# Kernel tuning notes

Measured on AMD Instinct MI355X. Metric: run time of the kernel, lower is better.

The kernel has to match this reference:

```python
import jax
import jax.numpy as jnp
from jax import lax
import numpy as np

NUM_OUTPUT_POINTS = 2048
NUM_NEIGHBORS = 32


def setup_inputs() -> dict:
    key = jax.random.key(0)
    k1, k2 = jax.random.split(key)
    coordinates = jax.random.normal(k1, (8, 8192, 3), dtype=jnp.float32)
    features = jax.random.normal(k2, (8, 8192, 128), dtype=jnp.float32)
    return {"coordinates": coordinates, "features": features}


def farthest_point_sample(coords, num_output_points):
    """Deterministic FPS (first point = index 0). coords: (B, N, D) -> idx (B, M) int32."""
    B, N, D = coords.shape

    def step(carry, _):
        dist, farthest = carry  # (B, N), (B,)
        centroid = jnp.take_along_axis(coords, farthest[:, None, None], axis=1)  # (B,1,D)
        cur = jnp.linalg.norm(coords - centroid, axis=-1)  # (B, N), L2 norm
        dist = jnp.minimum(dist, cur)
        new_far = jnp.argmax(dist, axis=-1).astype(jnp.int32)
        return (dist, new_far), farthest

    init = (jnp.full((B, N), 1e10, coords.dtype), jnp.zeros((B,), jnp.int32))
    _, idx = lax.scan(step, init, None, length=num_output_points)  # (M, B)
    return idx.T  # (B, M)


def knn_point(num_neighbors, coords, centers):
    """coords (B,N,D), centers (B,M,D) -> (B,M,K) indices of nearest neighbors (L2)."""
    # squared distances via expansion (avoids (B,M,N,D) diff tensor)
    c2 = jnp.sum(centers * centers, axis=-1, keepdims=True)        # (B,M,1)
    p2 = jnp.sum(coords * coords, axis=-1)[:, None, :]             # (B,1,N)
    d2 = c2 + p2 - 2.0 * jnp.einsum('bmd,bnd->bmn', centers, coords)
    _, nbr_idx = lax.top_k(-d2, num_neighbors)                     # smallest distances
    return nbr_idx


def _gather_points(points, idx):
    """points (B,N,C), idx (B,...) -> (B,...,C)."""
    return jax.vmap(lambda p, i: p[i])(points, idx)


def reference(coordinates, features):
    fps_idx = farthest_point_sample(coordinates, NUM_OUTPUT_POINTS)      # (B, M)
    out_coordinates = _gather_points(coordinates, fps_idx)               # (B, M, D)
    nbr_idx = knn_point(NUM_NEIGHBORS, coordinates, out_coordinates)     # (B, M, K)
    group_features = _gather_points(features, nbr_idx)                   # (B, M, K, C)
    out_features = jnp.mean(group_features, axis=2)                      # (B, M, C)
    return out_coordinates, out_features
```

## Files before the change

kernel.cpp:

```cpp
#include <hip/hip_runtime.h>

#define BB 8
#define NN 8192
#define MM 2048
#define KK 32
#define CC 128

#define FPS_T 512
#define FPS_P (NN / FPS_T)

template <int Ctrl, int RowMask>
__device__ __forceinline__ int dpp_i(int x) {
  return __builtin_amdgcn_update_dpp(x, x, Ctrl, RowMask, 0xf, false);
}

__device__ __forceinline__ float wave_max63(float v) {
  v = fmaxf(v, __int_as_float(dpp_i<0x111, 0xf>(__float_as_int(v))));
  v = fmaxf(v, __int_as_float(dpp_i<0x112, 0xf>(__float_as_int(v))));
  v = fmaxf(v, __int_as_float(dpp_i<0x114, 0xf>(__float_as_int(v))));
  v = fmaxf(v, __int_as_float(dpp_i<0x118, 0xf>(__float_as_int(v))));
  v = fmaxf(v, __int_as_float(dpp_i<0x142, 0xa>(__float_as_int(v))));
  v = fmaxf(v, __int_as_float(dpp_i<0x143, 0xc>(__float_as_int(v))));
  return v;
}

__device__ __forceinline__ unsigned int wave_minu63(unsigned int v) {
  unsigned int o;
  o = (unsigned int)dpp_i<0x111, 0xf>((int)v); v = o < v ? o : v;
  o = (unsigned int)dpp_i<0x112, 0xf>((int)v); v = o < v ? o : v;
  o = (unsigned int)dpp_i<0x114, 0xf>((int)v); v = o < v ? o : v;
  o = (unsigned int)dpp_i<0x118, 0xf>((int)v); v = o < v ? o : v;
  o = (unsigned int)dpp_i<0x142, 0xa>((int)v); v = o < v ? o : v;
  o = (unsigned int)dpp_i<0x143, 0xc>((int)v); v = o < v ? o : v;
  return v;
}

template <int Ctrl, int RowMask>
__device__ __forceinline__ unsigned long long dpp_u64(unsigned long long v) {
  const int lo = (int)(unsigned int)v;
  const int hi = (int)(unsigned int)(v >> 32);
  const unsigned int nlo = (unsigned int)dpp_i<Ctrl, RowMask>(lo);
  const unsigned int nhi = (unsigned int)dpp_i<Ctrl, RowMask>(hi);
  return ((unsigned long long)nhi << 32) | nlo;
}

__device__ __forceinline__ unsigned long long wave_minu64_63(unsigned long long v) {
  unsigned long long o;
  o = dpp_u64<0x111, 0xf>(v); v = o < v ? o : v;
  o = dpp_u64<0x112, 0xf>(v); v = o < v ? o : v;
  o = dpp_u64<0x114, 0xf>(v); v = o < v ? o : v;
  o = dpp_u64<0x118, 0xf>(v); v = o < v ? o : v;
  o = dpp_u64<0x142, 0xa>(v); v = o < v ? o : v;
  o = dpp_u64<0x143, 0xc>(v); v = o < v ? o : v;
  return v;
}

__global__ __launch_bounds__(FPS_T, 1)
void fps_kernel(const float* __restrict__ coords, float* __restrict__ out_coords) {
  const int b = blockIdx.x;
  const int t = threadIdx.x;
  const float* cb = coords + (size_t)b * NN * 3;

  __shared__ float s_x[NN], s_y[NN], s_z[NN];
  __shared__ float s_gpart[FPS_T / 64];
  __shared__ unsigned int s_ipart[FPS_T / 64];

  float x[FPS_P], y[FPS_P], z[FPS_P], d2m[FPS_P];
#pragma unroll
  for (int j = 0; j < FPS_P; ++j) {
    const int p = t + j * FPS_T;
    x[j] = cb[p * 3 + 0];
    y[j] = cb[p * 3 + 1];
    z[j] = cb[p * 3 + 2];
    d2m[j] = 1e20f;
    s_x[p] = x[j]; s_y[p] = y[j]; s_z[p] = z[j];
  }

  if (t == 0) {
    out_coords[(size_t)(b * MM) * 3 + 0] = cb[0];
    out_coords[(size_t)(b * MM) * 3 + 1] = cb[1];
    out_coords[(size_t)(b * MM) * 3 + 2] = cb[2];
  }
  float cx = cb[0], cy = cb[1], cz = cb[2];

  for (int it = 1; it < MM; ++it) {
    float bestv = -1.0f;
#pragma unroll
    for (int j = 0; j < FPS_P; ++j) {
      const float dx = __fsub_rn(x[j], cx);
      const float dy = __fsub_rn(y[j], cy);
      const float dz = __fsub_rn(z[j], cz);
      const float d2 = __fadd_rn(__fadd_rn(__fmul_rn(dx, dx), __fmul_rn(dy, dy)),
                                 __fmul_rn(dz, dz));
      const float nd = fminf(d2m[j], d2);
      d2m[j] = nd;
      bestv = fmaxf(bestv, nd);
    }

    const float wv = wave_max63(bestv);
    if ((t & 63) == 63) s_gpart[t >> 6] = wv;
    __syncthreads();
    float gmax = s_gpart[0];
#pragma unroll
    for (int w = 1; w < FPS_T / 64; ++w) gmax = fmaxf(gmax, s_gpart[w]);

    float lo_f;
    if (!(gmax > 0.0f)) {
      lo_f = 0.0f;
    } else {
      const float s = __fsqrt_rn(gmax);
      const float sp = __int_as_float(__float_as_int(s) - 1);
      const double mid = 0.5 * ((double)s + (double)sp);
      const double lod = mid * mid;
      float c = (float)lod;
      if ((double)c < lod) c = __int_as_float(__float_as_int(c) + 1);
      lo_f = c;
    }

    unsigned int mi = 0xFFFFFFFFu;
    if (bestv >= lo_f) {
#pragma unroll
      for (int j = 0; j < FPS_P; ++j) {
        const unsigned int pi = (unsigned int)(t + j * FPS_T);
        if (d2m[j] >= lo_f && pi < mi) mi = pi;
      }
    }
    const unsigned int wi = wave_minu63(mi);
    if ((t & 63) == 63) s_ipart[t >> 6] = wi;
    __syncthreads();
    unsigned int widx = s_ipart[0];
#pragma unroll
    for (int w = 1; w < FPS_T / 64; ++w) widx = s_ipart[w] < widx ? s_ipart[w] : widx;

    cx = s_x[widx]; cy = s_y[widx]; cz = s_z[widx];
    if (t == (it & (FPS_T - 1))) {
      float* oc = out_coords + ((size_t)b * MM + it) * 3;
      oc[0] = cx; oc[1] = cy; oc[2] = cz;
    }
  }
}

__global__ __launch_bounds__(256, 4)
void knn_mean_kernel(const float* __restrict__ coords,
                     const float* __restrict__ feats,
                     const float* __restrict__ out_coords,
                     float* __restrict__ out_feats) {
  const int q = blockIdx.x;
  const int b = q >> 11;
  const int t = threadIdx.x;
  const float* cb = coords + (size_t)b * NN * 3;

  const float cx = out_coords[(size_t)q * 3 + 0];
  const float cy = out_coords[(size_t)q * 3 + 1];
  const float cz = out_coords[(size_t)q * 3 + 2];
  const float c2 = __fadd_rn(__fadd_rn(__fmul_rn(cx, cx), __fmul_rn(cy, cy)),
                             __fmul_rn(cz, cz));

  unsigned long long key[32];
  unsigned long long lmin = ~0ULL;
#pragma unroll
  for (int j = 0; j < 32; ++j) {
    const int p = t + j * 256;
    const float px = cb[p * 3 + 0], py = cb[p * 3 + 1], pz = cb[p * 3 + 2];
    const float p2 = __fadd_rn(__fadd_rn(__fmul_rn(px, px), __fmul_rn(py, py)),
                               __fmul_rn(pz, pz));
    const float dot = __fmaf_rn(cz, pz, __fmaf_rn(cy, py, __fmul_rn(cx, px)));
    const float d2 = __fsub_rn(__fadd_rn(c2, p2), __fadd_rn(dot, dot));
    unsigned int ub = __float_as_uint(d2);
    ub ^= (((unsigned int)((int)ub >> 31)) | 0x80000000u);
    key[j] = ((unsigned long long)ub << 32) | (unsigned int)p;
    lmin = key[j] < lmin ? key[j] : lmin;
  }

  __shared__ unsigned long long s_pmin[2][4];
  __shared__ int s_nbr[KK];

  for (int r = 0; r < KK; ++r) {
    const unsigned long long wv = wave_minu64_63(lmin);
    if ((t & 63) == 63) s_pmin[r & 1][t >> 6] = wv;
    __syncthreads();

    const unsigned long long* pm = s_pmin[r & 1];
    unsigned long long g = pm[0];
    g = pm[1] < g ? pm[1] : g;
    g = pm[2] < g ? pm[2] : g;
    g = pm[3] < g ? pm[3] : g;
    const int widx = (int)(unsigned int)(g & 0xFFFFFFFFull);

    if (t == (widx & 255)) {
      unsigned long long nm = ~0ULL;
#pragma unroll
      for (int j = 0; j < 32; ++j) {
        key[j] = (key[j] == g) ? ~0ULL : key[j];
        nm = key[j] < nm ? key[j] : nm;
      }
      lmin = nm;
    }
    if (t == 0) s_nbr[r] = widx;
  }
  __syncthreads();

  const int c = t & (CC - 1);
  const int half = t >> 7;
  const float* fb = feats + (size_t)b * NN * CC;
  float s = 0.0f;
#pragma unroll
  for (int k = 0; k < 16; ++k) {
    const int p = s_nbr[half * 16 + k];
    s = __fadd_rn(s, fb[(size_t)p * CC + c]);
  }
  __shared__ float s_sum[CC];
  if (half == 1) s_sum[c] = s;
  __syncthreads();
  if (half == 0) {
    const float tot = __fadd_rn(s, s_sum[c]);
    out_feats[(size_t)q * CC + c] = tot * 0.03125f;
  }
}

extern "C" void kernel_launch(void* const* d_in, const int* in_sizes, int n_in,
                              void* d_out, int out_size, void* d_ws, size_t ws_size,
                              hipStream_t stream) {
  const float* coords = (const float*)d_in[0];
  const float* feats  = (const float*)d_in[1];
  float* out_coords = (float*)d_out;
  float* out_feats  = (float*)d_out + (size_t)BB * MM * 3;

  fps_kernel<<<BB, FPS_T, 0, stream>>>(coords, out_coords);
  knn_mean_kernel<<<BB * MM, 256, 0, stream>>>(coords, feats, out_coords,
                                               out_feats);
}
```

Measured before the change: 2.655 ms.

## Pack FPS/KNN argmin keys into doubles and skip the second FPS reduction

In the FPS loop each wave now tracks a packed (distance, index) top-1 plus the second-largest distance, reduced with double max via DPP. The second block-wide reduction and barrier run only when the runner-up falls within the rounding-tie window. The KNN kernel packs keys into non-negative doubles so min/compare use native f64 ops instead of emulated 64-bit integer compares. It also switches to contiguous per-thread float4 coordinate loads and removes keys by comparing against the previous winner. This adds extra per-step work (a second-max track, an index scan) and relies on the packed-double ordering matching the original tie-breaking.

```diff
diff --git a/kernel.cpp b/kernel.cpp
--- a/kernel.cpp
+++ b/kernel.cpp
@@ -1,4 +1,7 @@
 #include <hip/hip_runtime.h>
+
+typedef unsigned int u32;
+typedef unsigned long long u64;
 
 #define BB 8
 #define NN 8192
@@ -14,45 +17,37 @@
   return __builtin_amdgcn_update_dpp(x, x, Ctrl, RowMask, 0xf, false);
 }
 
-__device__ __forceinline__ float wave_max63(float v) {
-  v = fmaxf(v, __int_as_float(dpp_i<0x111, 0xf>(__float_as_int(v))));
-  v = fmaxf(v, __int_as_float(dpp_i<0x112, 0xf>(__float_as_int(v))));
-  v = fmaxf(v, __int_as_float(dpp_i<0x114, 0xf>(__float_as_int(v))));
-  v = fmaxf(v, __int_as_float(dpp_i<0x118, 0xf>(__float_as_int(v))));
-  v = fmaxf(v, __int_as_float(dpp_i<0x142, 0xa>(__float_as_int(v))));
-  v = fmaxf(v, __int_as_float(dpp_i<0x143, 0xc>(__float_as_int(v))));
+template <int Ctrl, int RowMask>
+__device__ __forceinline__ double dpp_d(double v) {
+  const u64 b = (u64)__double_as_longlong(v);
+  const int lo = dpp_i<Ctrl, RowMask>((int)(u32)b);
+  const int hi = dpp_i<Ctrl, RowMask>((int)(u32)(b >> 32));
+  return __longlong_as_double((long long)(((u64)(u32)hi << 32) | (u32)lo));
+}
+
+__device__ __forceinline__ u32 wave_minu63(u32 v) {
+  u32 o;
+  o = (u32)dpp_i<0x111, 0xf>((int)v); v = o < v ? o : v;
+  o = (u32)dpp_i<0x112, 0xf>((int)v); v = o < v ? o : v;
+  o = (u32)dpp_i<0x114, 0xf>((int)v); v = o < v ? o : v;
+  o = (u32)dpp_i<0x118, 0xf>((int)v); v = o < v ? o : v;
+  o = (u32)dpp_i<0x142, 0xa>((int)v); v = o < v ? o : v;
+  o = (u32)dpp_i<0x143, 0xc>((int)v); v = o < v ? o : v;
   return v;
 }
 
-__device__ __forceinline__ unsigned int wave_minu63(unsigned int v) {
-  unsigned int o;
-  o = (unsigned int)dpp_i<0x111, 0xf>((int)v); v = o < v ? o : v;
-  o = (unsigned int)dpp_i<0x112, 0xf>((int)v); v = o < v ? o : v;
-  o = (unsigned int)dpp_i<0x114, 0xf>((int)v); v = o < v ? o : v;
-  o = (unsigned int)dpp_i<0x118, 0xf>((int)v); v = o < v ? o : v;
-  o = (unsigned int)dpp_i<0x142, 0xa>((int)v); v = o < v ? o : v;
-  o = (unsigned int)dpp_i<0x143, 0xc>((int)v); v = o < v ? o : v;
+__device__ __forceinline__ double wave_minf64_63(double v) {
+  v = fmin(v, dpp_d<0x111, 0xf>(v));
+  v = fmin(v, dpp_d<0x112, 0xf>(v));
+  v = fmin(v, dpp_d<0x114, 0xf>(v));
+  v = fmin(v, dpp_d<0x118, 0xf>(v));
+  v = fmin(v, dpp_d<0x142, 0xa>(v));
+  v = fmin(v, dpp_d<0x143, 0xc>(v));
   return v;
 }
 
-template <int Ctrl, int RowMask>
-__device__ __forceinline__ unsigned long long dpp_u64(unsigned long long v) {
-  const int lo = (int)(unsigned int)v;
-  const int hi = (int)(unsigned int)(v >> 32);
-  const unsigned int nlo = (unsigned int)dpp_i<Ctrl, RowMask>(lo);
-  const unsigned int nhi = (unsigned int)dpp_i<Ctrl, RowMask>(hi);
-  return ((unsigned long long)nhi << 32) | nlo;
-}
-
-__device__ __forceinline__ unsigned long long wave_minu64_63(unsigned long long v) {
-  unsigned long long o;
-  o = dpp_u64<0x111, 0xf>(v); v = o < v ? o : v;
-  o = dpp_u64<0x112, 0xf>(v); v = o < v ? o : v;
-  o = dpp_u64<0x114, 0xf>(v); v = o < v ? o : v;
-  o = dpp_u64<0x118, 0xf>(v); v = o < v ? o : v;
-  o = dpp_u64<0x142, 0xa>(v); v = o < v ? o : v;
-  o = dpp_u64<0x143, 0xc>(v); v = o < v ? o : v;
-  return v;
+__device__ __forceinline__ float pk_d2(double p) {
+  return __uint_as_float((u32)(((u64)__double_as_longlong(p)) >> 31));
 }
 
 __global__ __launch_bounds__(FPS_T, 1)
@@ -62,8 +57,9 @@
   const float* cb = coords + (size_t)b * NN * 3;
 
   __shared__ float s_x[NN], s_y[NN], s_z[NN];
-  __shared__ float s_gpart[FPS_T / 64];
-  __shared__ unsigned int s_ipart[FPS_T / 64];
+  __shared__ double s_m1[2][FPS_T / 64];
+  __shared__ float s_m2[2][FPS_T / 64];
+  __shared__ u32 s_ri[2][FPS_T / 64];
 
   float x[FPS_P], y[FPS_P], z[FPS_P], d2m[FPS_P];
 #pragma unroll
@@ -84,7 +80,9 @@
   float cx = cb[0], cy = cb[1], cz = cb[2];
 
   for (int it = 1; it < MM; ++it) {
-    float bestv = -1.0f;
+    const int par = it & 1;
+
+    float tm1 = -1.0f, tm2 = -1.0f;
 #pragma unroll
     for (int j = 0; j < FPS_P; ++j) {
       const float dx = __fsub_rn(x[j], cx);
@@ -94,15 +92,56 @@
                                  __fmul_rn(dz, dz));
       const float nd = fminf(d2m[j], d2);
       d2m[j] = nd;
-      bestv = fmaxf(bestv, nd);
-    }
-
-    const float wv = wave_max63(bestv);
-    if ((t & 63) == 63) s_gpart[t >> 6] = wv;
+      const float lo = fminf(tm1, nd);
+      tm1 = fmaxf(tm1, nd);
+      tm2 = fmaxf(tm2, lo);
+    }
+
+    u32 mi = 0xFFFFFFFFu;
+#pragma unroll
+    for (int j = 0; j < FPS_P; ++j) {
+      const u32 pi = (u32)(t + j * FPS_T);
+      if (d2m[j] == tm1 && pi < mi) mi = pi;
+    }
+    double m1 = __longlong_as_double(
+        (long long)(((u64)__float_as_uint(tm1) << 31) | (u64)(8191u - mi)));
+    float m2 = tm2;
+
+#define FPS_T2_STEP(CTRL, MASK)                                              \
+  {                                                                          \
+    const double o1 = dpp_d<CTRL, MASK>(m1);                                 \
+    const float o2 = __int_as_float(dpp_i<CTRL, MASK>(__float_as_int(m2)));  \
+    const double lo2 = fmin(m1, o1);                                         \
+    m1 = fmax(m1, o1);                                                       \
+    m2 = fmaxf(fmaxf(m2, o2), pk_d2(lo2));                                   \
+  }
+    FPS_T2_STEP(0x111, 0xf)
+    FPS_T2_STEP(0x112, 0xf)
+    FPS_T2_STEP(0x114, 0xf)
+    FPS_T2_STEP(0x118, 0xf)
+    FPS_T2_STEP(0x142, 0xa)
+    FPS_T2_STEP(0x143, 0xc)
+#undef FPS_T2_STEP
+
+    if ((t & 63) == 63) {
+      s_m1[par][t >> 6] = m1;
+      s_m2[par][t >> 6] = m2;
+    }
     __syncthreads();
-    float gmax = s_gpart[0];
-#pragma unroll
-    for (int w = 1; w < FPS_T / 64; ++w) gmax = fmaxf(gmax, s_gpart[w]);
+
+    double g1 = s_m1[par][0];
+#pragma unroll
+    for (int w = 1; w < FPS_T / 64; ++w) g1 = fmax(g1, s_m1[par][w]);
+    float g2 = -1.0f;
+#pragma unroll
+    for (int w = 0; w < FPS_T / 64; ++w) {
+      const double pw = s_m1[par][w];
+      const float contrib = (pw == g1) ? s_m2[par][w] : pk_d2(pw);
+      g2 = fmaxf(g2, contrib);
+    }
+    const u64 g1b = (u64)__double_as_longlong(g1);
+    const float gmax = __uint_as_float((u32)(g1b >> 31));
+    const u32 cand = 8191u - (u32)(g1b & 0x1FFFull);
 
     float lo_f;
     if (!(gmax > 0.0f)) {
@@ -117,23 +156,29 @@
       lo_f = c;
     }
 
-    unsigned int mi = 0xFFFFFFFFu;
-    if (bestv >= lo_f) {
-#pragma unroll
-      for (int j = 0; j < FPS_P; ++j) {
-        const unsigned int pi = (unsigned int)(t + j * FPS_T);
-        if (d2m[j] >= lo_f && pi < mi) mi = pi;
+    u32 widx;
+    if (g2 < lo_f) {
+      widx = cand;
+    } else {
+      u32 ri = 0xFFFFFFFFu;
+      if (tm1 >= lo_f) {
+#pragma unroll
+        for (int j = 0; j < FPS_P; ++j) {
+          const u32 pi = (u32)(t + j * FPS_T);
+          if (d2m[j] >= lo_f && pi < ri) ri = pi;
+        }
       }
-    }
-    const unsigned int wi = wave_minu63(mi);
-    if ((t & 63) == 63) s_ipart[t >> 6] = wi;
-    __syncthreads();
-    unsigned int widx = s_ipart[0];
-#pragma unroll
-    for (int w = 1; w < FPS_T / 64; ++w) widx = s_ipart[w] < widx ? s_ipart[w] : widx;
+      const u32 wi = wave_minu63(ri);
+      if ((t & 63) == 63) s_ri[par][t >> 6] = wi;
+      __syncthreads();
+      widx = s_ri[par][0];
+#pragma unroll
+      for (int w = 1; w < FPS_T / 64; ++w)
+        widx = s_ri[par][w] < widx ? s_ri[par][w] : widx;
+    }
 
     cx = s_x[widx]; cy = s_y[widx]; cz = s_z[widx];
-    if (t == (it & (FPS_T - 1))) {
+    if (t == 0) {
       float* oc = out_coords + ((size_t)b * MM + it) * 3;
       oc[0] = cx; oc[1] = cy; oc[2] = cz;
     }
@@ -156,43 +201,54 @@
   const float c2 = __fadd_rn(__fadd_rn(__fmul_rn(cx, cx), __fmul_rn(cy, cy)),
                              __fmul_rn(cz, cz));
 
-  unsigned long long key[32];
-  unsigned long long lmin = ~0ULL;
-#pragma unroll
-  for (int j = 0; j < 32; ++j) {
-    const int p = t + j * 256;
-    const float px = cb[p * 3 + 0], py = cb[p * 3 + 1], pz = cb[p * 3 + 2];
-    const float p2 = __fadd_rn(__fadd_rn(__fmul_rn(px, px), __fmul_rn(py, py)),
-                               __fmul_rn(pz, pz));
-    const float dot = __fmaf_rn(cz, pz, __fmaf_rn(cy, py, __fmul_rn(cx, px)));
-    const float d2 = __fsub_rn(__fadd_rn(c2, p2), __fadd_rn(dot, dot));
-    unsigned int ub = __float_as_uint(d2);
-    ub ^= (((unsigned int)((int)ub >> 31)) | 0x80000000u);
-    key[j] = ((unsigned long long)ub << 32) | (unsigned int)p;
-    lmin = key[j] < lmin ? key[j] : lmin;
-  }
-
-  __shared__ unsigned long long s_pmin[2][4];
+  const double HUGE_SENT = __longlong_as_double(0x7FE0000000000000LL);
+  double key[32];
+  double lmin = HUGE_SENT;
+  const float* tb = cb + t * 96;
+
+#pragma unroll
+  for (int ch = 0; ch < 8; ++ch) {
+    const float4 q0 = *(const float4*)(tb + ch * 12 + 0);
+    const float4 q1 = *(const float4*)(tb + ch * 12 + 4);
+    const float4 q2 = *(const float4*)(tb + ch * 12 + 8);
+    const float pxs[4] = {q0.x, q0.w, q1.z, q2.y};
+    const float pys[4] = {q0.y, q1.x, q1.w, q2.z};
+    const float pzs[4] = {q0.z, q1.y, q2.x, q2.w};
+#pragma unroll
+    for (int k = 0; k < 4; ++k) {
+      const int j = ch * 4 + k;
+      const int p = t * 32 + j;
+      const float px = pxs[k], py = pys[k], pz = pzs[k];
+      const float p2 = __fadd_rn(__fadd_rn(__fmul_rn(px, px), __fmul_rn(py, py)),
+                                 __fmul_rn(pz, pz));
+      const float dot = __fmaf_rn(cz, pz, __fmaf_rn(cy, py, __fmul_rn(cx, px)));
+      const float d2 = __fsub_rn(__fadd_rn(c2, p2), __fadd_rn(dot, dot));
+      u32 ub = __float_as_uint(d2);
+      ub ^= (((u32)((int)ub >> 31)) | 0x80000000u);
+      key[j] = __longlong_as_double(
+          (long long)(((u64)ub << 31) | (u32)p));
+      lmin = fmin(lmin, key[j]);
+    }
+  }
+
+  __shared__ double s_pmin[2][4];
   __shared__ int s_nbr[KK];
 
   for (int r = 0; r < KK; ++r) {
-    const unsigned long long wv = wave_minu64_63(lmin);
+    const double wv = wave_minf64_63(lmin);
     if ((t & 63) == 63) s_pmin[r & 1][t >> 6] = wv;
     __syncthreads();
 
-    const unsigned long long* pm = s_pmin[r & 1];
-    unsigned long long g = pm[0];
-    g = pm[1] < g ? pm[1] : g;
-    g = pm[2] < g ? pm[2] : g;
-    g = pm[3] < g ? pm[3] : g;
-    const int widx = (int)(unsigned int)(g & 0xFFFFFFFFull);
-
-    if (t == (widx & 255)) {
-      unsigned long long nm = ~0ULL;
+    const double* pm = s_pmin[r & 1];
+    const double g = fmin(fmin(pm[0], pm[1]), fmin(pm[2], pm[3]));
+    const int widx = (int)((u64)__double_as_longlong(g) & 0x1FFFull);
+
+    if (t == (widx >> 5)) {
+      double nm = HUGE_SENT;
 #pragma unroll
       for (int j = 0; j < 32; ++j) {
-        key[j] = (key[j] == g) ? ~0ULL : key[j];
-        nm = key[j] < nm ? key[j] : nm;
+        const double sel = (key[j] > g) ? key[j] : HUGE_SENT;
+        nm = fmin(nm, sel);
       }
       lmin = nm;
     }
```

Measured after the change: 3.475 ms. +30.9%, slower.

## Replace iterative KNN min-extraction with radix-select histogram; pack FPS math

Applied to the files above, without the earlier changes.

Top-32 selection in the KNN kernel changes from 32 rounds of block-wide 64-bit min reductions to a 4-pass 12/11-bit radix select over a shared-memory histogram keyed on distance and index. Matching indices are then compacted with an atomic counter. The neighbours are summed in a different order, so floating-point rounding of the mean may change. Coordinates are now loaded contiguously per thread with float4 reads, and FPS distance updates use packed v_pk_add/mul_f32 on pairs of points.

```diff
diff --git a/kernel.cpp b/kernel.cpp
--- a/kernel.cpp
+++ b/kernel.cpp
@@ -1,4 +1,8 @@
 #include <hip/hip_runtime.h>
+
+typedef unsigned int u32;
+typedef unsigned long long u64;
+typedef float f32x2 __attribute__((ext_vector_type(2)));
 
 #define BB 8
 #define NN 8192
@@ -7,53 +11,50 @@
 #define CC 128
 
 #define FPS_T 512
-#define FPS_P (NN / FPS_T)
+#define FPS_PAIRS 8
 
 template <int Ctrl, int RowMask>
-__device__ __forceinline__ int dpp_i(int x) {
+__device__ __forceinline__ int dpp_mov(int x) {
   return __builtin_amdgcn_update_dpp(x, x, Ctrl, RowMask, 0xf, false);
 }
+template <int Ctrl, int RowMask>
+__device__ __forceinline__ u32 dpp_scan_add(u32 x) {
+  return x + (u32)__builtin_amdgcn_update_dpp(0, (int)x, Ctrl, RowMask, 0xf, false);
+}
 
 __device__ __forceinline__ float wave_max63(float v) {
-  v = fmaxf(v, __int_as_float(dpp_i<0x111, 0xf>(__float_as_int(v))));
-  v = fmaxf(v, __int_as_float(dpp_i<0x112, 0xf>(__float_as_int(v))));
-  v = fmaxf(v, __int_as_float(dpp_i<0x114, 0xf>(__float_as_int(v))));
-  v = fmaxf(v, __int_as_float(dpp_i<0x118, 0xf>(__float_as_int(v))));
-  v = fmaxf(v, __int_as_float(dpp_i<0x142, 0xa>(__float_as_int(v))));
-  v = fmaxf(v, __int_as_float(dpp_i<0x143, 0xc>(__float_as_int(v))));
+  v = fmaxf(v, __int_as_float(dpp_mov<0x111, 0xf>(__float_as_int(v))));
+  v = fmaxf(v, __int_as_float(dpp_mov<0x112, 0xf>(__float_as_int(v))));
+  v = fmaxf(v, __int_as_float(dpp_mov<0x114, 0xf>(__float_as_int(v))));
+  v = fmaxf(v, __int_as_float(dpp_mov<0x118, 0xf>(__float_as_int(v))));
+  v = fmaxf(v, __int_as_float(dpp_mov<0x142, 0xa>(__float_as_int(v))));
+  v = fmaxf(v, __int_as_float(dpp_mov<0x143, 0xc>(__float_as_int(v))));
   return v;
 }
 
-__device__ __forceinline__ unsigned int wave_minu63(unsigned int v) {
-  unsigned int o;
-  o = (unsigned int)dpp_i<0x111, 0xf>((int)v); v = o < v ? o : v;
-  o = (unsigned int)dpp_i<0x112, 0xf>((int)v); v = o < v ? o : v;
-  o = (unsigned int)dpp_i<0x114, 0xf>((int)v); v = o < v ? o : v;
-  o = (unsigned int)dpp_i<0x118, 0xf>((int)v); v = o < v ? o : v;
-  o = (unsigned int)dpp_i<0x142, 0xa>((int)v); v = o < v ? o : v;
-  o = (unsigned int)dpp_i<0x143, 0xc>((int)v); v = o < v ? o : v;
+__device__ __forceinline__ u32 wave_minu63(u32 v) {
+  u32 o;
+  o = (u32)dpp_mov<0x111, 0xf>((int)v); v = o < v ? o : v;
+  o = (u32)dpp_mov<0x112, 0xf>((int)v); v = o < v ? o : v;
+  o = (u32)dpp_mov<0x114, 0xf>((int)v); v = o < v ? o : v;
+  o = (u32)dpp_mov<0x118, 0xf>((int)v); v = o < v ? o : v;
+  o = (u32)dpp_mov<0x142, 0xa>((int)v); v = o < v ? o : v;
+  o = (u32)dpp_mov<0x143, 0xc>((int)v); v = o < v ? o : v;
   return v;
 }
 
-template <int Ctrl, int RowMask>
-__device__ __forceinline__ unsigned long long dpp_u64(unsigned long long v) {
-  const int lo = (int)(unsigned int)v;
-  const int hi = (int)(unsigned int)(v >> 32);
-  const unsigned int nlo = (unsigned int)dpp_i<Ctrl, RowMask>(lo);
-  const unsigned int nhi = (unsigned int)dpp_i<Ctrl, RowMask>(hi);
-  return ((unsigned long long)nhi << 32) | nlo;
-}
-
-__device__ __forceinline__ unsigned long long wave_minu64_63(unsigned long long v) {
-  unsigned long long o;
-  o = dpp_u64<0x111, 0xf>(v); v = o < v ? o : v;
-  o = dpp_u64<0x112, 0xf>(v); v = o < v ? o : v;
-  o = dpp_u64<0x114, 0xf>(v); v = o < v ? o : v;
-  o = dpp_u64<0x118, 0xf>(v); v = o < v ? o : v;
-  o = dpp_u64<0x142, 0xa>(v); v = o < v ? o : v;
-  o = dpp_u64<0x143, 0xc>(v); v = o < v ? o : v;
-  return v;
-}
+__device__ __forceinline__ u32 wave_scan_incl(u32 x) {
+  x = dpp_scan_add<0x111, 0xf>(x);
+  x = dpp_scan_add<0x112, 0xf>(x);
+  x = dpp_scan_add<0x114, 0xf>(x);
+  x = dpp_scan_add<0x118, 0xf>(x);
+  x = dpp_scan_add<0x142, 0xa>(x);
+  x = dpp_scan_add<0x143, 0xc>(x);
+  return x;
+}
+
+#define PK_ADD(d, a, b) asm("v_pk_add_f32 %0, %1, %2" : "=v"(d) : "v"(a), "v"(b))
+#define PK_MUL(d, a, b) asm("v_pk_mul_f32 %0, %1, %2" : "=v"(d) : "v"(a), "v"(b))
 
 __global__ __launch_bounds__(FPS_T, 1)
 void fps_kernel(const float* __restrict__ coords, float* __restrict__ out_coords) {
@@ -63,17 +64,20 @@
 
   __shared__ float s_x[NN], s_y[NN], s_z[NN];
   __shared__ float s_gpart[FPS_T / 64];
-  __shared__ unsigned int s_ipart[FPS_T / 64];
-
-  float x[FPS_P], y[FPS_P], z[FPS_P], d2m[FPS_P];
-#pragma unroll
-  for (int j = 0; j < FPS_P; ++j) {
-    const int p = t + j * FPS_T;
-    x[j] = cb[p * 3 + 0];
-    y[j] = cb[p * 3 + 1];
-    z[j] = cb[p * 3 + 2];
-    d2m[j] = 1e20f;
-    s_x[p] = x[j]; s_y[p] = y[j]; s_z[p] = z[j];
+  __shared__ u32 s_ipart[FPS_T / 64];
+
+  f32x2 x[FPS_PAIRS], y[FPS_PAIRS], z[FPS_PAIRS], d2m[FPS_PAIRS];
+#pragma unroll
+  for (int k = 0; k < FPS_PAIRS; ++k) {
+    const int p0 = t + (2 * k) * FPS_T;
+    const int p1 = t + (2 * k + 1) * FPS_T;
+    x[k].x = cb[p0 * 3 + 0]; x[k].y = cb[p1 * 3 + 0];
+    y[k].x = cb[p0 * 3 + 1]; y[k].y = cb[p1 * 3 + 1];
+    z[k].x = cb[p0 * 3 + 2]; z[k].y = cb[p1 * 3 + 2];
+    d2m[k].x = 1e20f; d2m[k].y = 1e20f;
+    s_x[p0] = x[k].x; s_x[p1] = x[k].y;
+    s_y[p0] = y[k].x; s_y[p1] = y[k].y;
+    s_z[p0] = z[k].x; s_z[p1] = z[k].y;
   }
 
   if (t == 0) {
@@ -84,18 +88,25 @@
   float cx = cb[0], cy = cb[1], cz = cb[2];
 
   for (int it = 1; it < MM; ++it) {
-    float bestv = -1.0f;
-#pragma unroll
-    for (int j = 0; j < FPS_P; ++j) {
-      const float dx = __fsub_rn(x[j], cx);
-      const float dy = __fsub_rn(y[j], cy);
-      const float dz = __fsub_rn(z[j], cz);
-      const float d2 = __fadd_rn(__fadd_rn(__fmul_rn(dx, dx), __fmul_rn(dy, dy)),
-                                 __fmul_rn(dz, dz));
-      const float nd = fminf(d2m[j], d2);
-      d2m[j] = nd;
-      bestv = fmaxf(bestv, nd);
-    }
+    const f32x2 ncx = {-cx, -cx}, ncy = {-cy, -cy}, ncz = {-cz, -cz};
+    f32x2 bv = {-1.0f, -1.0f};
+#pragma unroll
+    for (int k = 0; k < FPS_PAIRS; ++k) {
+      f32x2 dx, dy, dz, t0, t1, t2, d2;
+      PK_ADD(dx, x[k], ncx);
+      PK_ADD(dy, y[k], ncy);
+      PK_ADD(dz, z[k], ncz);
+      PK_MUL(t0, dx, dx);
+      PK_MUL(t1, dy, dy);
+      PK_ADD(t0, t0, t1);
+      PK_MUL(t2, dz, dz);
+      PK_ADD(d2, t0, t2);
+      d2m[k].x = fminf(d2m[k].x, d2.x);
+      d2m[k].y = fminf(d2m[k].y, d2.y);
+      bv.x = fmaxf(bv.x, d2m[k].x);
+      bv.y = fmaxf(bv.y, d2m[k].y);
+    }
+    const float bestv = fmaxf(bv.x, bv.y);
 
     const float wv = wave_max63(bestv);
     if ((t & 63) == 63) s_gpart[t >> 6] = wv;
@@ -117,20 +128,23 @@
       lo_f = c;
     }
 
-    unsigned int mi = 0xFFFFFFFFu;
+    u32 mi = 0xFFFFFFFFu;
     if (bestv >= lo_f) {
 #pragma unroll
-      for (int j = 0; j < FPS_P; ++j) {
-        const unsigned int pi = (unsigned int)(t + j * FPS_T);
-        if (d2m[j] >= lo_f && pi < mi) mi = pi;
+      for (int k = 0; k < FPS_PAIRS; ++k) {
+        const u32 p0 = (u32)(t + (2 * k) * FPS_T);
+        const u32 p1 = (u32)(t + (2 * k + 1) * FPS_T);
+        if (d2m[k].x >= lo_f && p0 < mi) mi = p0;
+        if (d2m[k].y >= lo_f && p1 < mi) mi = p1;
       }
     }
-    const unsigned int wi = wave_minu63(mi);
+    const u32 wi = wave_minu63(mi);
     if ((t & 63) == 63) s_ipart[t >> 6] = wi;
     __syncthreads();
-    unsigned int widx = s_ipart[0];
-#pragma unroll
-    for (int w = 1; w < FPS_T / 64; ++w) widx = s_ipart[w] < widx ? s_ipart[w] : widx;
+    u32 widx = s_ipart[0];
+#pragma unroll
+    for (int w = 1; w < FPS_T / 64; ++w)
+      widx = s_ipart[w] < widx ? s_ipart[w] : widx;
 
     cx = s_x[widx]; cy = s_y[widx]; cz = s_z[widx];
     if (t == (it & (FPS_T - 1))) {
@@ -156,47 +170,118 @@
   const float c2 = __fadd_rn(__fadd_rn(__fmul_rn(cx, cx), __fmul_rn(cy, cy)),
                              __fmul_rn(cz, cz));
 
-  unsigned long long key[32];
-  unsigned long long lmin = ~0ULL;
+  u32 D[32];
+  const float* tb = cb + t * 96;
+#pragma unroll
+  for (int ch = 0; ch < 8; ++ch) {
+    const float4 q0 = *(const float4*)(tb + ch * 12 + 0);
+    const float4 q1 = *(const float4*)(tb + ch * 12 + 4);
+    const float4 q2 = *(const float4*)(tb + ch * 12 + 8);
+    const float pxs[4] = {q0.x, q0.w, q1.z, q2.y};
+    const float pys[4] = {q0.y, q1.x, q1.w, q2.z};
+    const float pzs[4] = {q0.z, q1.y, q2.x, q2.w};
+#pragma unroll
+    for (int kk = 0; kk < 4; ++kk) {
+      const int j = ch * 4 + kk;
+      const float px = pxs[kk], py = pys[kk], pz = pzs[kk];
+      const float p2 = __fadd_rn(__fadd_rn(__fmul_rn(px, px), __fmul_rn(py, py)),
+                                 __fmul_rn(pz, pz));
+      const float dot = __fmaf_rn(cz, pz, __fmaf_rn(cy, py, __fmul_rn(cx, px)));
+      const float d2 = __fsub_rn(__fadd_rn(c2, p2), __fadd_rn(dot, dot));
+      u32 ub = __float_as_uint(d2);
+      ub ^= (((u32)((int)ub >> 31)) | 0x80000000u);
+      D[j] = ub;
+    }
+  }
+
+  __shared__ u32 s_hist[4096];
+  __shared__ u32 s_wsum[4];
+  __shared__ u32 s_bin, s_r, s_full;
+  __shared__ u32 s_cnt;
+  __shared__ int s_nbr[KK];
+  __shared__ float s_sum[CC];
+
+  const int w = t >> 6;
+  u64 hi = 0;
+  u32 k_rem = KK;
+  u64 thr = 0;
+  bool done = false;
+
+  constexpr int SHIFT[4] = {33, 22, 11, 0};
+  constexpr int SBITS[4] = {45, 33, 22, 11};
+
+#pragma unroll
+  for (int p = 0; p < 4; ++p) {
+    if (!done) {
+      const uint4 z4 = {0u, 0u, 0u, 0u};
+#pragma unroll
+      for (int i = 0; i < 4; ++i) *(uint4*)&s_hist[t * 16 + i * 4] = z4;
+      __syncthreads();
+
+#pragma unroll
+      for (int j = 0; j < 32; ++j) {
+        const u64 key = ((u64)D[j] << 13) | (u32)(t * 32 + j);
+        if ((key >> SBITS[p]) == hi)
+          atomicAdd(&s_hist[(u32)(key >> SHIFT[p]) & 4095u], 1u);
+      }
+      __syncthreads();
+
+      const uint4 h0 = *(const uint4*)&s_hist[t * 16 + 0];
+      const uint4 h1 = *(const uint4*)&s_hist[t * 16 + 4];
+      const uint4 h2 = *(const uint4*)&s_hist[t * 16 + 8];
+      const uint4 h3 = *(const uint4*)&s_hist[t * 16 + 12];
+      const u32 ls = h0.x + h0.y + h0.z + h0.w + h1.x + h1.y + h1.z + h1.w +
+                     h2.x + h2.y + h2.z + h2.w + h3.x + h3.y + h3.z + h3.w;
+      const u32 incl = wave_scan_incl(ls);
+      if ((t & 63) == 63) s_wsum[w] = incl;
+      __syncthreads();
+      u32 base = 0;
+      if (w > 0) base += s_wsum[0];
+      if (w > 1) base += s_wsum[1];
+      if (w > 2) base += s_wsum[2];
+      const u32 pre_grp = base + incl - ls;
+
+      if (pre_grp < k_rem && k_rem <= pre_grp + ls) {
+        const u32 hh[16] = {h0.x, h0.y, h0.z, h0.w, h1.x, h1.y, h1.z, h1.w,
+                            h2.x, h2.y, h2.z, h2.w, h3.x, h3.y, h3.z, h3.w};
+        u32 c = pre_grp;
+#pragma unroll
+        for (int i = 0; i < 16; ++i) {
+          const u32 h = hh[i];
+          if (k_rem > c && k_rem <= c + h) {
+            s_bin = (u32)(t * 16 + i);
+            s_r = k_rem - c;
+            s_full = (k_rem - c == h) ? 1u : 0u;
+          }
+          c += h;
+        }
+      }
+      __syncthreads();
+
+      const u32 bin = s_bin;
+      const u32 r = s_r;
+      const u32 fullf = s_full;
+      hi = (hi << (SBITS[p] - SHIFT[p])) | bin;
+      if (fullf) {
+        thr = (SHIFT[p] > 0)
+                  ? ((hi << SHIFT[p]) | ((1ULL << SHIFT[p]) - 1ULL))
+                  : hi;
+        done = true;
+      } else {
+        k_rem = r;
+      }
+    }
+  }
+
+  if (t == 0) s_cnt = 0;
+  __syncthreads();
 #pragma unroll
   for (int j = 0; j < 32; ++j) {
-    const int p = t + j * 256;
-    const float px = cb[p * 3 + 0], py = cb[p * 3 + 1], pz = cb[p * 3 + 2];
-    const float p2 = __fadd_rn(__fadd_rn(__fmul_rn(px, px), __fmul_rn(py, py)),
-                               __fmul_rn(pz, pz));
-    const float dot = __fmaf_rn(cz, pz, __fmaf_rn(cy, py, __fmul_rn(cx, px)));
-    const float d2 = __fsub_rn(__fadd_rn(c2, p2), __fadd_rn(dot, dot));
-    unsigned int ub = __float_as_uint(d2);
-    ub ^= (((unsigned int)((int)ub >> 31)) | 0x80000000u);
-    key[j] = ((unsigned long long)ub << 32) | (unsigned int)p;
-    lmin = key[j] < lmin ? key[j] : lmin;
-  }
-
-  __shared__ unsigned long long s_pmin[2][4];
-  __shared__ int s_nbr[KK];
-
-  for (int r = 0; r < KK; ++r) {
-    const unsigned long long wv = wave_minu64_63(lmin);
-    if ((t & 63) == 63) s_pmin[r & 1][t >> 6] = wv;
-    __syncthreads();
-
-    const unsigned long long* pm = s_pmin[r & 1];
-    unsigned long long g = pm[0];
-    g = pm[1] < g ? pm[1] : g;
-    g = pm[2] < g ? pm[2] : g;
-    g = pm[3] < g ? pm[3] : g;
-    const int widx = (int)(unsigned int)(g & 0xFFFFFFFFull);
-
-    if (t == (widx & 255)) {
-      unsigned long long nm = ~0ULL;
-#pragma unroll
-      for (int j = 0; j < 32; ++j) {
-        key[j] = (key[j] == g) ? ~0ULL : key[j];
-        nm = key[j] < nm ? key[j] : nm;
-      }
-      lmin = nm;
-    }
-    if (t == 0) s_nbr[r] = widx;
+    const u64 key = ((u64)D[j] << 13) | (u32)(t * 32 + j);
+    if (key <= thr) {
+      const u32 pos = atomicAdd(&s_cnt, 1u);
+      s_nbr[pos] = t * 32 + j;
+    }
   }
   __syncthreads();
 
@@ -209,7 +294,6 @@
     const int p = s_nbr[half * 16 + k];
     s = __fadd_rn(s, fb[(size_t)p * CC + c]);
   }
-  __shared__ float s_sum[CC];
   if (half == 1) s_sum[c] = s;
   __syncthreads();
   if (half == 0) {
```

Measured after the change: 2.499 ms. 1.06x faster.
